# Optimization experiments

Measured on AMD Instinct MI355X. Metric: run time of the kernel, lower is better.

Reference implementation:

```python
import jax, jax.numpy as jnp
import numpy as np

D, N = 512, 256          # transition steps, batch
H, L, V = 128, 64, 32000 # h_dim, label_dim, lexicon_size


def _valid_transitions(seed=0):
    # generate a valid shift/reduce schedule: reduce only when stack depth >= 2
    rng = np.random.default_rng(seed)
    ptr = np.zeros(N, np.int64)
    trans = np.zeros((D, N), np.int32)
    for t in range(D):
        r = ((rng.random(N) < 0.6) & (ptr >= 2)).astype(np.int32)
        trans[t] = r
        ptr += 1 - 2 * r  # every step pushes 1; reduce pops 2 first
    return jnp.asarray(trans)


def setup_inputs() -> dict:
    key = jax.random.key(0)
    k1, k2, k3 = jax.random.split(key, 3)
    transitions = _valid_transitions()
    labels_idx = jax.random.randint(k1, (D, N), 0, V, dtype=jnp.int32)
    emb = jax.random.normal(k2, (V, L), jnp.float32) * 0.02
    emb = emb.at[0].set(0.0)  # padding_idx=0
    arg_dim = L + 2 * H
    W = jax.random.normal(k3, (arg_dim, 5 * H), jnp.float32) / np.sqrt(arg_dim).astype(np.float32)
    b = jnp.zeros((5 * H,), jnp.float32)
    leaf = jnp.zeros((H,), jnp.float32)  # leaf_input placeholder vector
    return {"transitions": transitions, "labels_idx": labels_idx,
            "emb": emb, "W": W, "b": b, "leaf": leaf}


def _cell(x, hl, hr, cl, cr, W, b):
    # binary TreeLSTM (Tai et al.): gates from concat(label, h_left, h_right)
    g = jnp.concatenate([x, hl, hr], axis=-1) @ W + b  # [N, 5H]
    i, fl, fr, o, u = jnp.split(g, 5, axis=-1)
    c = jax.nn.sigmoid(i) * jnp.tanh(u) + jax.nn.sigmoid(fl) * cl + jax.nn.sigmoid(fr) * cr
    h = jax.nn.sigmoid(o) * jnp.tanh(c)
    return c, h


def reference(transitions, labels_idx, emb, W, b, leaf):
    labels = emb[labels_idx]  # [D,N,L]
    bidx = jnp.arange(N)

    def step(carry, inp):
        h_st, c_st, idx_st, ptr = carry  # [D,N,H],[D,N,H],[D,N],[N]
        t, mask, lab = inp
        mf = mask.astype(bool)[:, None]
        # right popped first, then left (matches _get_indices call order)
        ridx = idx_st[(ptr - 1) % D, bidx]
        lidx = idx_st[(ptr - 2) % D, bidx]
        hl = jnp.where(mf, h_st[lidx, bidx], leaf)
        hr = jnp.where(mf, h_st[ridx, bidx], leaf)
        cl = jnp.where(mf, c_st[lidx, bidx], leaf)
        cr = jnp.where(mf, c_st[ridx, bidx], leaf)
        c, h = _cell(lab, hl, hr, cl, cr, W, b)
        h_st = h_st.at[t].set(h)   # embeddings_stack[step] = h
        c_st = c_st.at[t].set(c)   # cells_stack[step] = c
        newptr = ptr - 2 * mask    # pops (if reduce)
        idx_st = idx_st.at[newptr, bidx].set(t)  # push current step for all batch
        return (h_st, c_st, idx_st, newptr + 1), None

    h_st = jnp.zeros((D, N, H), jnp.float32)
    c_st = jnp.zeros((D, N, H), jnp.float32)
    idx_st = jnp.zeros((D, N), jnp.int32)
    ptr = jnp.zeros((N,), jnp.int32)
    (h_st, c_st, _, _), _ = jax.lax.scan(
        step, (h_st, c_st, idx_st, ptr),
        (jnp.arange(D, dtype=jnp.int32), transitions, labels))
    # original returns (thin_stack[1][D-1], thin_stack[0][D-1]) = (cells, embeddings)
    return c_st[D - 1], h_st[D - 1]
```

## Files before the change

kernel.cpp:

```cpp
#include <hip/hip_runtime.h>
#include <stdint.h>


#define D     512
#define HD    128
#define LD    64
#define NTHR  512
#define GPR   328

typedef unsigned long long u64t;

__device__ __forceinline__ float sigf(float x){ return 1.0f/(1.0f+__expf(-x)); }
__device__ __forceinline__ float tanh_(float x){ return 1.0f-2.0f/(__expf(2.0f*x)+1.0f); }
__device__ __forceinline__ u64t gld64(const float* p){
  return __hip_atomic_load((const u64t*)p, __ATOMIC_RELAXED, __HIP_MEMORY_SCOPE_AGENT);
}
__device__ __forceinline__ u64t gld64r(const u64t* p){
  return __hip_atomic_load(p, __ATOMIC_RELAXED, __HIP_MEMORY_SCOPE_AGENT);
}
__device__ __forceinline__ void gst32(float* p, float v){
  __hip_atomic_store(p, v, __ATOMIC_RELAXED, __HIP_MEMORY_SCOPE_AGENT);
}
__device__ __forceinline__ void gst64r(u64t* p, u64t v){
  __hip_atomic_store(p, v, __ATOMIC_RELAXED, __HIP_MEMORY_SCOPE_AGENT);
}
__device__ __forceinline__ u64t packw(float v, unsigned tg){
  return ((u64t)tg << 32) | (u64t)__float_as_uint(v);
}
__device__ __forceinline__ float loww(u64t w){
  return __uint_as_float((unsigned)(w & 0xffffffffu));
}

__global__ __launch_bounds__(NTHR,2) void spinn_kernel(
    const int* __restrict__ trans, const int* __restrict__ labels,
    const float* __restrict__ emb, const float* __restrict__ W,
    const float* __restrict__ bias, const float* __restrict__ leaf,
    float* __restrict__ out, u64t* __restrict__ mail,
    float* __restrict__ rec, float* __restrict__ cown)
{
  const int bid = blockIdx.x;
  const int g2 = ((bid>>4)<<3) | (bid&7);
  const int sl = (bid>>3)&1, ps = sl^1;
  const int gb0 = g2*2;
  const int tid = threadIdx.x;
  const int kg = tid>>6, lane = tid&63;
  const int cq = lane;

  __shared__ __align__(16) float xs[2][2][320];
  __shared__ __align__(16) float gpq[16][GPR];
  __shared__ float bsl[640];
  __shared__ float lshd[HD];
  __shared__ float clb[2][2][HD];
  __shared__ uint8_t mS[D][2];
  __shared__ short liA[D][2];
  __shared__ unsigned short stk_[2][D];

  float4 wr4[40]; float wr1[40];
  {
    const int gq = (cq>>4)*128 + sl*64 + ((cq*4)&63);
    const int gu = 512 + sl*64 + cq;
#pragma unroll
    for (int j=0;j<40;++j){
      int k = kg*40 + j;
      wr4[j] = *(const float4*)(W + (size_t)k*640 + gq);
      wr1[j] = W[(size_t)k*640 + gu];
    }
  }
  for (int c = tid; c < 640; c += NTHR) bsl[c] = bias[c];
  if (tid < HD) lshd[tid] = leaf[tid];
  if (tid < 2){
    int b = tid, p = 0;
    for (int t=0;t<D;++t){
      int m = trans[t*256 + gb0 + b];
      short li = 0;
      if (m) li = (short)stk_[b][p-2];
      mS[t][b] = (uint8_t)m; liA[t][b] = li;
      int np = p - 2*m; stk_[b][np] = (unsigned short)t; p = np+1;
    }
  }
  __syncthreads();

  for (int idx = tid; idx < 640; idx += NTHR){
    int b = (idx >= 320) ? 1 : 0;
    int r = idx - b*320;
    if (r < 64){
      int row = labels[gb0 + b];
      xs[0][b][r] = emb[(size_t)row*LD + r];
    } else {
      xs[0][b][r] = lshd[(r-64)&127];
    }
  }
  __syncthreads();

  auto gemm = [&](int cur){
    float4 a0 = {0.f,0.f,0.f,0.f}, a1 = {0.f,0.f,0.f,0.f};
    float u0 = 0.f, u1 = 0.f;
#pragma unroll
    for (int j4=0;j4<10;++j4){
      int k = kg*40 + j4*4;
      float4 x0 = *(const float4*)&xs[cur][0][k];
      float4 x1 = *(const float4*)&xs[cur][1][k];
      float xa0[4] = {x0.x,x0.y,x0.z,x0.w};
      float xa1[4] = {x1.x,x1.y,x1.z,x1.w};
#pragma unroll
      for (int jj=0;jj<4;++jj){
        float4 w = wr4[j4*4+jj];
        float wu = wr1[j4*4+jj];
        a0.x = __builtin_fmaf(w.x, xa0[jj], a0.x);
        a0.y = __builtin_fmaf(w.y, xa0[jj], a0.y);
        a0.z = __builtin_fmaf(w.z, xa0[jj], a0.z);
        a0.w = __builtin_fmaf(w.w, xa0[jj], a0.w);
        a1.x = __builtin_fmaf(w.x, xa1[jj], a1.x);
        a1.y = __builtin_fmaf(w.y, xa1[jj], a1.y);
        a1.z = __builtin_fmaf(w.z, xa1[jj], a1.z);
        a1.w = __builtin_fmaf(w.w, xa1[jj], a1.w);
        u0 = __builtin_fmaf(wu, xa0[jj], u0);
        u1 = __builtin_fmaf(wu, xa1[jj], u1);
      }
    }
    *(float4*)&gpq[kg*2+0][cq*4] = a0;
    *(float4*)&gpq[kg*2+1][cq*4] = a1;
    gpq[kg*2+0][256+cq] = u0;
    gpq[kg*2+1][256+cq] = u1;
  };

  float ccprev = 0.f;

  for (int t=0;t<D;++t){
    const int cur = t&1, nxt = cur^1;

    gemm(cur);
    __syncthreads();

    {
      u64t* mo = mail + (((size_t)(t&3)*128 + g2)*2 + sl)*640;
      {
        const int w = tid;
        const int b = (w >= 320), c = w - b*320;
        float a = 0.f;
#pragma unroll
        for (int kk=0; kk<8; ++kk) a += gpq[kk*2+b][c];
        gst64r(mo + w, packw(a, (unsigned)(t+1)));
      }
      if (tid < 128){
        const int w = 512 + tid;
        const int c = w - 320;
        float a = 0.f;
#pragma unroll
        for (int kk=0; kk<8; ++kk) a += gpq[kk*2+1][c];
        gst64r(mo + w, packw(a, (unsigned)(t+1)));
      }
    }

    if (tid < 256){
      const int b = tid>>7, h = tid&127, dl = h&63;
      const int own = ((h>>6) == sl);
      const int m = mS[t][b];
      float s[5];
      if (own){
#pragma unroll
        for (int g=0; g<5; ++g){
          const int c = (g<4) ? (g*64+dl) : (256+dl);
          float a = 0.f;
#pragma unroll
          for (int kk=0; kk<8; ++kk) a += gpq[kk*2+b][c];
          s[g] = a;
        }
      } else {
        const u64t* mi = mail + (((size_t)(t&3)*128 + g2)*2 + ps)*640 + b*320;
        const unsigned want = (unsigned)(t+1);
        u64t pw[5];
#pragma unroll
        for (int g=0;g<4;++g) pw[g] = gld64r(mi + g*64 + dl);
        pw[4] = gld64r(mi + 256 + dl);
        int it = 0;
        while (!__all(((unsigned)(pw[0]>>32) == want) &
                      ((unsigned)(pw[1]>>32) == want) &
                      ((unsigned)(pw[2]>>32) == want) &
                      ((unsigned)(pw[3]>>32) == want) &
                      ((unsigned)(pw[4]>>32) == want))){
          if (it >= 4) __builtin_amdgcn_s_sleep(1);
#pragma unroll
          for (int g=0;g<4;++g) pw[g] = gld64r(mi + g*64 + dl);
          pw[4] = gld64r(mi + 256 + dl);
          if (++it > (1<<17)) break;
        }
#pragma unroll
        for (int g=0;g<5;++g) s[g] = loww(pw[g]);
      }
#pragma unroll
      for (int g=0;g<4;++g) s[g] += bsl[g*128 + h];
      s[4] += bsl[512 + h];

      const float cl_ = m ? clb[cur][b][h] : lshd[h];
      const float cr_ = m ? ccprev : lshd[h];
      const float cc = sigf(s[0])*tanh_(s[4]) + sigf(s[1])*cl_ + sigf(s[2])*cr_;
      const float hh = sigf(s[3])*tanh_(cc);
      ccprev = cc;

      if (sl == 0){
        const size_t ro = (((size_t)t*128 + g2)*2 + b)*HD + h;
        gst32(rec + ro, hh);
        gst32(cown + ro, cc);
      }
      if (t == D-1){
        out[(size_t)(gb0+b)*HD + h] = cc;
        out[(size_t)256*HD + (size_t)(gb0+b)*HD + h] = hh;
      } else {
        xs[nxt][b][192+h] = mS[t+1][b] ? hh : lshd[h];
      }
      if (t+2 < D && mS[t+2][b] && liA[t+2][b] == t){
        xs[cur][b][64+h] = hh;
        clb[cur][b][h]   = cc;
      }
    } else if (tid < 384){
      if (t+1 < D){
        const int idx = tid-256, b = idx>>6, jj = idx&63, h2 = jj*2;
        const int m1 = mS[t+1][b]; const int li = liA[t+1][b];
        if (m1){
          if (li <= t-2){
            const size_t ro = (((size_t)li*128 + g2)*2 + b)*HD + h2;
            union{u64t u; float f[2];} h_, c_;
            h_.u = gld64(rec + ro);
            c_.u = gld64(cown + ro);
            xs[nxt][b][64+h2]   = h_.f[0];
            xs[nxt][b][64+h2+1] = h_.f[1];
            clb[nxt][b][h2]     = c_.f[0];
            clb[nxt][b][h2+1]   = c_.f[1];
          }
        } else {
          xs[nxt][b][64+h2]   = lshd[h2];
          xs[nxt][b][64+h2+1] = lshd[h2+1];
          clb[nxt][b][h2]     = lshd[h2];
          clb[nxt][b][h2+1]   = lshd[h2+1];
        }
      }
    } else {
      if (t+1 < D){
        const int idx = tid-384, b = idx>>6, jj = idx&63;
        const int row = labels[(t+1)*256 + gb0 + b];
        xs[nxt][b][jj] = emb[(size_t)row*LD + jj];
      }
    }
    __syncthreads();
  }
}

extern "C" void kernel_launch(void* const* d_in, const int* in_sizes, int n_in,
                              void* d_out, int out_size, void* d_ws, size_t ws_size,
                              hipStream_t stream) {
  (void)in_sizes; (void)n_in; (void)out_size; (void)ws_size;
  const int*   trans  = (const int*)d_in[0];
  const int*   labels = (const int*)d_in[1];
  const float* emb    = (const float*)d_in[2];
  const float* W      = (const float*)d_in[3];
  const float* bias   = (const float*)d_in[4];
  const float* leaf   = (const float*)d_in[5];
  float* out = (float*)d_out;

  uint8_t* ws = (uint8_t*)d_ws;
  u64t*  mail = (u64t*)ws;
  float* rec  = (float*)(ws + ((size_t)8<<20));
  float* cown = (float*)(ws + ((size_t)72<<20));

  spinn_kernel<<<dim3(256), dim3(NTHR), 0, stream>>>(
      trans, labels, emb, W, bias, leaf, out, mail, rec, cown);
}
```

Before: 1.710 ms.

## Defer partner-half cell update into next step's GEMM to hide mailbox latency

Reorders the K dimension of W so the part of h that depends on the partner block's half lands in a separate slice of the GEMM. The partner-half cell computation, which needs mailbox polling across blocks, now runs one step later inside warps 6 and 7. Those warps compute the GEMM slices that do not depend on it first, and a workgroup flag orders the rest. This aims to take the cross-block mailbox wait off the critical path between steps, at the cost of more complex intra-block synchronization, warp imbalance, and an extra epilogue.

```diff
diff --git a/kernel.cpp b/kernel.cpp
--- a/kernel.cpp
+++ b/kernel.cpp
@@ -29,6 +29,14 @@
 }
 __device__ __forceinline__ float loww(u64t w){
   return __uint_as_float((unsigned)(w & 0xffffffffu));
+}
+__device__ __forceinline__ int permrow(int k, int sl){
+  const int ps = sl^1;
+  if (k < 64)  return k;
+  if (k < 128) return 64  + sl*64 + (k-64);
+  if (k < 192) return 64  + ps*64 + (k-128);
+  if (k < 256) return 192 + sl*64 + (k-192);
+  return 192 + ps*64 + (k-256);
 }
 
 __global__ __launch_bounds__(NTHR,2) void spinn_kernel(
@@ -54,6 +62,7 @@
   __shared__ uint8_t mS[D][2];
   __shared__ short liA[D][2];
   __shared__ unsigned short stk_[2][D];
+  __shared__ int f6[2];
 
   float4 wr4[40]; float wr1[40];
   {
@@ -61,13 +70,14 @@
     const int gu = 512 + sl*64 + cq;
 #pragma unroll
     for (int j=0;j<40;++j){
-      int k = kg*40 + j;
-      wr4[j] = *(const float4*)(W + (size_t)k*640 + gq);
-      wr1[j] = W[(size_t)k*640 + gu];
+      const int R = permrow(kg*40 + j, sl);
+      wr4[j] = *(const float4*)(W + (size_t)R*640 + gq);
+      wr1[j] = W[(size_t)R*640 + gu];
     }
   }
   for (int c = tid; c < 640; c += NTHR) bsl[c] = bias[c];
   if (tid < HD) lshd[tid] = leaf[tid];
+  if (tid == 0){ f6[0] = 0; f6[1] = 0; }
   if (tid < 2){
     int b = tid, p = 0;
     for (int t=0;t<D;++t){
@@ -81,22 +91,22 @@
   __syncthreads();
 
   for (int idx = tid; idx < 640; idx += NTHR){
-    int b = (idx >= 320) ? 1 : 0;
-    int r = idx - b*320;
-    if (r < 64){
-      int row = labels[gb0 + b];
-      xs[0][b][r] = emb[(size_t)row*LD + r];
-    } else {
-      xs[0][b][r] = lshd[(r-64)&127];
-    }
+    const int b = (idx >= 320) ? 1 : 0;
+    const int r = idx - b*320;
+    float v;
+    if (r < 64)       v = emb[(size_t)labels[gb0 + b]*LD + r];
+    else if (r < 128) v = lshd[sl*64 + (r-64)];
+    else if (r < 192) v = lshd[ps*64 + (r-128)];
+    else if (r < 256) v = lshd[sl*64 + (r-192)];
+    else              v = lshd[ps*64 + (r-256)];
+    xs[0][b][r] = v;
   }
   __syncthreads();
 
-  auto gemm = [&](int cur){
-    float4 a0 = {0.f,0.f,0.f,0.f}, a1 = {0.f,0.f,0.f,0.f};
-    float u0 = 0.f, u1 = 0.f;
-#pragma unroll
-    for (int j4=0;j4<10;++j4){
+  auto gemmr = [&](int cur, int j0, int j1,
+                   float4& a0, float4& a1, float& u0, float& u1){
+#pragma unroll
+    for (int j4=j0;j4<j1;++j4){
       int k = kg*40 + j4*4;
       float4 x0 = *(const float4*)&xs[cur][0][k];
       float4 x1 = *(const float4*)&xs[cur][1][k];
@@ -118,18 +128,83 @@
         u1 = __builtin_fmaf(wu, xa1[jj], u1);
       }
     }
-    *(float4*)&gpq[kg*2+0][cq*4] = a0;
-    *(float4*)&gpq[kg*2+1][cq*4] = a1;
-    gpq[kg*2+0][256+cq] = u0;
-    gpq[kg*2+1][256+cq] = u1;
   };
 
   float ccprev = 0.f;
+  float ccp67  = 0.f;
+
+  auto deferCell = [&](int b, int dl, int t, int cur, int nxt){
+    const int pd = ps*64 + dl;
+    const u64t* mi = mail + (((size_t)((t-1)&3)*128 + g2)*2 + ps)*640 + b*320;
+    const unsigned want = (unsigned)t;
+    u64t pw[5]; int it = 0;
+    for (;;){
+#pragma unroll
+      for (int g=0;g<4;++g) pw[g] = gld64r(mi + g*64 + dl);
+      pw[4] = gld64r(mi + 256 + dl);
+      if (__all(((unsigned)(pw[0]>>32) == want) &
+                ((unsigned)(pw[1]>>32) == want) &
+                ((unsigned)(pw[2]>>32) == want) &
+                ((unsigned)(pw[3]>>32) == want) &
+                ((unsigned)(pw[4]>>32) == want))) break;
+      if (it >= 4) __builtin_amdgcn_s_sleep(1);
+      if (++it > (1<<17)) break;
+    }
+    float s[5];
+#pragma unroll
+    for (int g=0;g<4;++g) s[g] = loww(pw[g]) + bsl[g*128 + pd];
+    s[4] = loww(pw[4]) + bsl[512 + pd];
+    const int m = mS[t-1][b];
+    const float cl_ = m ? clb[nxt][b][pd] : lshd[pd];
+    const float cr_ = m ? ccp67 : lshd[pd];
+    const float cc = sigf(s[0])*tanh_(s[4]) + sigf(s[1])*cl_ + sigf(s[2])*cr_;
+    const float hh = sigf(s[3])*tanh_(cc);
+    ccp67 = cc;
+    xs[cur][b][256+dl] = mS[t][b] ? hh : lshd[pd];
+    if (t+1 < D && mS[t+1][b] && liA[t+1][b] == t-1){
+      xs[nxt][b][128+dl] = hh;
+      clb[nxt][b][pd]    = cc;
+    }
+    if (sl == 0){
+      const size_t ro = (((size_t)(t-1)*128 + g2)*2 + b)*HD + pd;
+      gst32(rec + ro, hh);
+      gst32(cown + ro, cc);
+    }
+  };
 
   for (int t=0;t<D;++t){
     const int cur = t&1, nxt = cur^1;
 
-    gemm(cur);
+    {
+      float4 a0 = {0.f,0.f,0.f,0.f}, a1 = {0.f,0.f,0.f,0.f};
+      float u0 = 0.f, u1 = 0.f;
+
+      if (kg <= 5){
+        gemmr(cur, 0, 10, a0, a1, u0, u1);
+      } else if (kg == 6){
+        gemmr(cur, 0, 4, a0, a1, u0, u1);
+        if (t > 0) deferCell(lane>>5, lane&31, t, cur, nxt);
+        if (lane == 0)
+          __hip_atomic_store(&f6[cur], t+1, __ATOMIC_RELEASE,
+                             __HIP_MEMORY_SCOPE_WORKGROUP);
+        gemmr(cur, 4, 10, a0, a1, u0, u1);
+      } else {
+        if (t > 0){
+          deferCell(lane>>5, 32+(lane&31), t, cur, nxt);
+          int it = 0;
+          while (__hip_atomic_load(&f6[cur], __ATOMIC_ACQUIRE,
+                                   __HIP_MEMORY_SCOPE_WORKGROUP) < t+1){
+            __builtin_amdgcn_s_sleep(1);
+            if (++it > (1<<17)) break;
+          }
+        }
+        gemmr(cur, 0, 10, a0, a1, u0, u1);
+      }
+      *(float4*)&gpq[kg*2+0][cq*4] = a0;
+      *(float4*)&gpq[kg*2+1][cq*4] = a1;
+      gpq[kg*2+0][256+cq] = u0;
+      gpq[kg*2+1][256+cq] = u1;
+    }
     __syncthreads();
 
     {
@@ -152,97 +227,101 @@
       }
     }
 
-    if (tid < 256){
-      const int b = tid>>7, h = tid&127, dl = h&63;
-      const int own = ((h>>6) == sl);
+    if (tid < 128){
+      const int b = tid>>6, dl = tid&63, gd = sl*64+dl;
       const int m = mS[t][b];
       float s[5];
-      if (own){
-#pragma unroll
-        for (int g=0; g<5; ++g){
-          const int c = (g<4) ? (g*64+dl) : (256+dl);
-          float a = 0.f;
-#pragma unroll
-          for (int kk=0; kk<8; ++kk) a += gpq[kk*2+b][c];
-          s[g] = a;
-        }
-      } else {
-        const u64t* mi = mail + (((size_t)(t&3)*128 + g2)*2 + ps)*640 + b*320;
-        const unsigned want = (unsigned)(t+1);
-        u64t pw[5];
-#pragma unroll
-        for (int g=0;g<4;++g) pw[g] = gld64r(mi + g*64 + dl);
-        pw[4] = gld64r(mi + 256 + dl);
-        int it = 0;
-        while (!__all(((unsigned)(pw[0]>>32) == want) &
-                      ((unsigned)(pw[1]>>32) == want) &
-                      ((unsigned)(pw[2]>>32) == want) &
-                      ((unsigned)(pw[3]>>32) == want) &
-                      ((unsigned)(pw[4]>>32) == want))){
-          if (it >= 4) __builtin_amdgcn_s_sleep(1);
-#pragma unroll
-          for (int g=0;g<4;++g) pw[g] = gld64r(mi + g*64 + dl);
-          pw[4] = gld64r(mi + 256 + dl);
-          if (++it > (1<<17)) break;
-        }
-#pragma unroll
-        for (int g=0;g<5;++g) s[g] = loww(pw[g]);
-      }
-#pragma unroll
-      for (int g=0;g<4;++g) s[g] += bsl[g*128 + h];
-      s[4] += bsl[512 + h];
-
-      const float cl_ = m ? clb[cur][b][h] : lshd[h];
-      const float cr_ = m ? ccprev : lshd[h];
+#pragma unroll
+      for (int g=0; g<5; ++g){
+        const int c = (g<4) ? (g*64+dl) : (256+dl);
+        float a = 0.f;
+#pragma unroll
+        for (int kk=0; kk<8; ++kk) a += gpq[kk*2+b][c];
+        s[g] = a + ((g<4) ? bsl[g*128 + gd] : bsl[512 + gd]);
+      }
+      const float cl_ = m ? clb[cur][b][gd] : lshd[gd];
+      const float cr_ = m ? ccprev : lshd[gd];
       const float cc = sigf(s[0])*tanh_(s[4]) + sigf(s[1])*cl_ + sigf(s[2])*cr_;
       const float hh = sigf(s[3])*tanh_(cc);
       ccprev = cc;
-
       if (sl == 0){
-        const size_t ro = (((size_t)t*128 + g2)*2 + b)*HD + h;
+        const size_t ro = (((size_t)t*128 + g2)*2 + b)*HD + gd;
         gst32(rec + ro, hh);
         gst32(cown + ro, cc);
       }
       if (t == D-1){
-        out[(size_t)(gb0+b)*HD + h] = cc;
-        out[(size_t)256*HD + (size_t)(gb0+b)*HD + h] = hh;
+        out[(size_t)(gb0+b)*HD + gd] = cc;
+        out[(size_t)256*HD + (size_t)(gb0+b)*HD + gd] = hh;
       } else {
-        xs[nxt][b][192+h] = mS[t+1][b] ? hh : lshd[h];
+        xs[nxt][b][192+dl] = mS[t+1][b] ? hh : lshd[gd];
       }
       if (t+2 < D && mS[t+2][b] && liA[t+2][b] == t){
-        xs[cur][b][64+h] = hh;
-        clb[cur][b][h]   = cc;
+        xs[cur][b][64+dl] = hh;
+        clb[cur][b][gd]   = cc;
+      }
+    } else if (tid < 256){
+      if (t+1 < D){
+        const int idx = tid-128, b = idx>>6, jj = idx&63;
+        const int row = labels[(t+1)*256 + gb0 + b];
+        xs[nxt][b][jj] = emb[(size_t)row*LD + jj];
       }
     } else if (tid < 384){
       if (t+1 < D){
         const int idx = tid-256, b = idx>>6, jj = idx&63, h2 = jj*2;
         const int m1 = mS[t+1][b]; const int li = liA[t+1][b];
+        const int s0 = ((h2>>6) == sl) ? (64 + (h2 & 63)) : (128 + (h2 & 63));
         if (m1){
           if (li <= t-2){
             const size_t ro = (((size_t)li*128 + g2)*2 + b)*HD + h2;
             union{u64t u; float f[2];} h_, c_;
             h_.u = gld64(rec + ro);
             c_.u = gld64(cown + ro);
-            xs[nxt][b][64+h2]   = h_.f[0];
-            xs[nxt][b][64+h2+1] = h_.f[1];
-            clb[nxt][b][h2]     = c_.f[0];
-            clb[nxt][b][h2+1]   = c_.f[1];
+            xs[nxt][b][s0]   = h_.f[0];
+            xs[nxt][b][s0+1] = h_.f[1];
+            clb[nxt][b][h2]   = c_.f[0];
+            clb[nxt][b][h2+1] = c_.f[1];
           }
         } else {
-          xs[nxt][b][64+h2]   = lshd[h2];
-          xs[nxt][b][64+h2+1] = lshd[h2+1];
-          clb[nxt][b][h2]     = lshd[h2];
-          clb[nxt][b][h2+1]   = lshd[h2+1];
+          xs[nxt][b][s0]   = lshd[h2];
+          xs[nxt][b][s0+1] = lshd[h2+1];
+          clb[nxt][b][h2]   = lshd[h2];
+          clb[nxt][b][h2+1] = lshd[h2+1];
         }
       }
-    } else {
-      if (t+1 < D){
-        const int idx = tid-384, b = idx>>6, jj = idx&63;
-        const int row = labels[(t+1)*256 + gb0 + b];
-        xs[nxt][b][jj] = emb[(size_t)row*LD + jj];
-      }
     }
     __syncthreads();
+  }
+
+  if (kg >= 6){
+    const int b = lane>>5;
+    const int dl = (kg==6) ? (lane&31) : (32 + (lane&31));
+    const int pd = ps*64 + dl;
+    const u64t* mi = mail + (((size_t)((D-1)&3)*128 + g2)*2 + ps)*640 + b*320;
+    const unsigned want = (unsigned)D;
+    u64t pw[5]; int it = 0;
+    for (;;){
+#pragma unroll
+      for (int g=0;g<4;++g) pw[g] = gld64r(mi + g*64 + dl);
+      pw[4] = gld64r(mi + 256 + dl);
+      if (__all(((unsigned)(pw[0]>>32) == want) &
+                ((unsigned)(pw[1]>>32) == want) &
+                ((unsigned)(pw[2]>>32) == want) &
+                ((unsigned)(pw[3]>>32) == want) &
+                ((unsigned)(pw[4]>>32) == want))) break;
+      if (it >= 4) __builtin_amdgcn_s_sleep(1);
+      if (++it > (1<<17)) break;
+    }
+    float s[5];
+#pragma unroll
+    for (int g=0;g<4;++g) s[g] = loww(pw[g]) + bsl[g*128 + pd];
+    s[4] = loww(pw[4]) + bsl[512 + pd];
+    const int m = mS[D-1][b];
+    const float cl_ = m ? clb[(D-1)&1][b][pd] : lshd[pd];
+    const float cr_ = m ? ccp67 : lshd[pd];
+    const float cc = sigf(s[0])*tanh_(s[4]) + sigf(s[1])*cl_ + sigf(s[2])*cr_;
+    const float hh = sigf(s[3])*tanh_(cc);
+    out[(size_t)(gb0+b)*HD + pd] = cc;
+    out[(size_t)256*HD + (size_t)(gb0+b)*HD + pd] = hh;
   }
 }
 
```

After: 3.123 ms. 1.83x slower.
